# Optimization experiments

Hardware: AMD Instinct MI355X
Metric: run time of the kernel (lower is better)

## Reference

```python
import jax, jax.numpy as jnp
import numpy as np

# Dimensions (see shape_source): B batches, W walks, L walk length, N anonymized node-id space
B, W, L, N = 256, 128, 20, 64
SIGMA = 2.0  # CooccurrenceMatrix(sigma=2.0)


def setup_inputs() -> dict:
    key = jax.random.key(0)
    k1, k2 = jax.random.split(key)
    anonymized_nodes = jax.random.randint(k1, (B, W, L), 0, N, dtype=jnp.int32)
    walk_masks = jax.random.randint(k2, (B, W, L), 0, 2).astype(bool)
    # Gaussian positional kernel buffer: kernel[i,j] = exp(-(i-j)^2 / sigma^2)
    pos = jnp.arange(L, dtype=jnp.float32)
    kernel = jnp.exp(-((pos[:, None] - pos[None, :]) ** 2) / (SIGMA ** 2))
    return {"anonymized_nodes": anonymized_nodes, "walk_masks": walk_masks, "kernel": kernel}


def reference(anonymized_nodes, walk_masks, kernel):
    # Faithful vectorized form of CooccurrenceMatrix.forward.
    # Original: per batch, group valid (walk,pos) entries by node id (sort +
    # change-points); for each group with >=2 entries, scatter-add
    # kernel[pos_i, pos_j] into cooccurrence[b, walk_i, walk_j] for all pairs
    # (i,j) in the group (including i==j). Then normalize by outer product of
    # walk lengths, clamp, tanh.
    valid = walk_masks.astype(jnp.float32)                     # [B,W,L]
    # T[b,w,l,n] = 1 if entry (w,l) is valid and holds node id n
    T = jax.nn.one_hot(anonymized_nodes, N, dtype=jnp.float32) * valid[..., None]  # [B,W,L,N]
    # Segments with < 2 occurrences contribute nothing (original skips them)
    cnt = T.sum(axis=(1, 2))                                   # [B,N]
    T = T * (cnt >= 2.0).astype(jnp.float32)[:, None, None, :]
    K = jnp.clip(kernel, -10.0, 10.0)                          # clamp as in _add_segment_deterministic
    # cooccurrence[b,w,v] = sum_n sum_{l,m} T[b,w,l,n] K[l,m] T[b,v,m,n]
    S = jnp.einsum('bwln,lm->bwmn', T, K)                      # [B,W,L,N]
    cooc = jnp.einsum('bwmn,bvmn->bwv', S, T)                  # [B,W,W]
    # Normalization by walk-length outer product
    walk_lens = valid.sum(-1)                                  # [B,W]
    norm = jnp.clip(walk_lens[:, :, None] * walk_lens[:, None, :], 1e-6, None)
    valid_pairs = (walk_lens[:, :, None] > 0) & (walk_lens[:, None, :] > 0)
    cooc = jnp.where(valid_pairs, cooc / norm, 0.0)
    return jnp.tanh(jnp.clip(cooc, -10.0, 10.0))
```

## Files before the change

kernel.cpp:

```cpp
#include <hip/hip_runtime.h>
#include <hip/hip_bf16.h>

#define BB   256
#define W    128
#define L    20
#define NN   64
#define WL   (W * L)
#define NT   1024
#define CS   129
#define NSLOT 3
#define NKEY (L * NN)

__global__ __launch_bounds__(NT) void cooc_kernel(
    const int* __restrict__ nodes,
    const void* __restrict__ masks,
    const float* __restrict__ kern,
    float* __restrict__ out)
{
    __shared__ __align__(16) float cooc[W * CS];
    __shared__ unsigned ent[WL + 4];
    __shared__ unsigned hist[NKEY];
    __shared__ int cnt[NN];
    __shared__ int wlen[W];
    __shared__ int det[3];
    __shared__ int totS;

    const int tid = threadIdx.x;
    const int b = blockIdx.x;
    const int base = b * WL;

    const unsigned mword = ((const unsigned*)masks)[tid];
    int nval[NSLOT];
    #pragma unroll
    for (int k = 0; k < NSLOT; k++) {
        int e = tid + k * NT;
        nval[k] = (e < WL) ? nodes[base + e] : 0;
    }

    if (tid < 3) det[tid] = 0;
    if (tid < W) wlen[tid] = 0;
    if (tid < NKEY) hist[tid] = 0;
    if (tid + NT < NKEY) hist[tid + NT] = 0;
    {
        float4* c4 = (float4*)cooc;
        for (int i = tid; i < (W * CS) / 4; i += NT)
            c4[i] = make_float4(0.f, 0.f, 0.f, 0.f);
    }
    {
        unsigned v = mword;
        unsigned long long b0 = __ballot(v > 1u);
        unsigned long long b1 = __ballot(v != 0u && v != 0x3F800000u);
        unsigned long long b2 = __ballot(v != 0u && v != 0x3F80u && v != 0x3F800000u &&
                                         v != 0x3F803F80u && v != 0x3C00u &&
                                         v != 0x3C000000u && v != 0x3C003C00u);
        if ((tid & 63) == 0) {
            if (b0) atomicOr(&det[0], 1);
            if (b1) atomicOr(&det[1], 1);
            if (b2) atomicOr(&det[2], 1);
        }
    }
    __syncthreads();
    const int flag = det[0] ? (det[1] ? (det[2] ? 1 : 3) : 2) : 0;

    auto validAt = [&](int idx) -> bool {
        switch (flag) {
            case 0:  return ((const int*)masks)[idx] != 0;
            case 2:  return ((const float*)masks)[idx] != 0.0f;
            case 3:  return ((const unsigned short*)masks)[idx] != 0;
            default: return ((const unsigned char*)masks)[idx] != 0;
        }
    };

    unsigned eval[NSLOT];
    int      kreg[NSLOT];
    #pragma unroll
    for (int k = 0; k < NSLOT; k++) {
        int e = tid + k * NT;
        eval[k] = 0xFFFFFFFFu;
        kreg[k] = 0;
        if (e < WL && validAt(base + e)) {
            int n = nval[k] & (NN - 1);
            int w = e / L;
            int l = e - w * L;
            eval[k] = ((unsigned)n << 12) | ((unsigned)l << 7) | (unsigned)w;
            kreg[k] = l * NN + n;
            atomicAdd(&hist[kreg[k]], 1u);
            atomicAdd(&wlen[w], 1);
        }
    }
    __syncthreads();

    if (tid < NN) {
        int s = 0;
        #pragma unroll
        for (int l = 0; l < L; l++) s += (int)hist[l * NN + tid];
        cnt[tid] = s;
        int inc = s;
        #pragma unroll
        for (int d = 1; d < NN; d <<= 1) {
            int t = __shfl_up(inc, d, 64);
            if (tid >= d) inc += t;
        }
        int run = inc - s;
        if (tid == NN - 1) totS = inc;
        #pragma unroll
        for (int l = 0; l < L; l++) {
            int t = (int)hist[l * NN + tid];
            hist[l * NN + tid] = (unsigned)run;
            run += t;
        }
    }
    __syncthreads();

    if (tid == 0) ent[totS] = 0xFFFFFFFFu;
    #pragma unroll
    for (int k = 0; k < NSLOT; k++) {
        if (eval[k] != 0xFFFFFFFFu) {
            unsigned p = atomicAdd(&hist[kreg[k]], 1u);
            ent[p] = eval[k];
        }
    }
    __syncthreads();

    const float KC = -0.360673760222f;
    const int tot = totS;
    #pragma unroll
    for (int k = 0; k < NSLOT; k++) {
        const int p = tid + k * NT;
        if (p >= tot) continue;
        const unsigned e = ent[p];
        const unsigned key1 = e >> 7;
        const int n = (int)(e >> 12);
        const int w1row = (int)(e & 127u) * CS;
        if (cnt[n] >= 2)
            atomicAdd(&cooc[w1row + (int)(e & 127u)], 0.5f);
        int j = p + 1;
        while (true) {
            unsigned e2 = ent[j];
            unsigned d = (e2 >> 7) - key1;
            if (d > 7u) break;
            float kv = __builtin_amdgcn_exp2f((float)(d * d) * KC);
            atomicAdd(&cooc[w1row + (int)(e2 & 127u)], kv);
            j++;
        }
    }
    __syncthreads();

    for (int i = tid; i < W * W; i += NT) {
        int wr = i >> 7;
        int v = i & (W - 1);
        float s = cooc[wr * CS + v] + cooc[v * CS + wr];
        int lw = wlen[wr], lv = wlen[v];
        float nrm = (float)(lw * lv);
        float x = s * __builtin_amdgcn_rcpf(fmaxf(nrm, 1e-6f));
        x = fminf(fmaxf(x, -10.f), 10.f);
        float e = __builtin_amdgcn_exp2f(x * 2.885390082f);
        float t = (e - 1.f) * __builtin_amdgcn_rcpf(e + 1.f);
        out[b * W * W + i] = (lw > 0 && lv > 0) ? t : 0.f;
    }
}

extern "C" void kernel_launch(void* const* d_in, const int* in_sizes, int n_in,
                              void* d_out, int out_size, void* d_ws, size_t ws_size,
                              hipStream_t stream) {
    const int*   nodes = (const int*)d_in[0];
    const void*  masks = d_in[1];
    const float* kern  = (const float*)d_in[2];
    float* out = (float*)d_out;

    cooc_kernel<<<BB, NT, 0, stream>>>(nodes, masks, kern, out);
}
```

Measured before the change: 82.03 us.

## Narrow the positional window and drop redundant atomics in the bucket scatter

The pair loop now uses a precomputed bucket end index and stops at a position difference of 5 instead of 7. This discards kernel terms of about exp(-9) and below, cutting the shared-memory atomic adds in the hot loop. The second atomic pass for the counting-sort scatter is gone: each entry keeps the rank it got from its first histogram atomic and adds a separate prefix offset. Walk lengths now come from ballot bitmasks and popcount instead of per-entry atomics. The trade is a slightly larger approximation error from the narrower window.

```diff
diff --git a/kernel.cpp b/kernel.cpp
--- a/kernel.cpp
+++ b/kernel.cpp
@@ -10,6 +10,7 @@
 #define CS   129
 #define NSLOT 3
 #define NKEY (L * NN)
+#define DLMAX 5
 
 __global__ __launch_bounds__(NT) void cooc_kernel(
     const int* __restrict__ nodes,
@@ -18,8 +19,10 @@
     float* __restrict__ out)
 {
     __shared__ __align__(16) float cooc[W * CS];
-    __shared__ unsigned ent[WL + 4];
+    __shared__ unsigned ent[WL];
     __shared__ unsigned hist[NKEY];
+    __shared__ unsigned offs[NKEY];
+    __shared__ unsigned long long maskS[40];
     __shared__ int cnt[NN];
     __shared__ int wlen[W];
     __shared__ int det[3];
@@ -38,8 +41,7 @@
     }
 
     if (tid < 3) det[tid] = 0;
-    if (tid < W) wlen[tid] = 0;
-    if (tid < NKEY) hist[tid] = 0;
+    hist[tid] = 0;
     if (tid + NT < NKEY) hist[tid + NT] = 0;
     {
         float4* c4 = (float4*)cooc;
@@ -73,20 +75,25 @@
 
     unsigned eval[NSLOT];
     int      kreg[NSLOT];
+    unsigned plocal[NSLOT];
     #pragma unroll
     for (int k = 0; k < NSLOT; k++) {
         int e = tid + k * NT;
+        bool valid = (e < WL) && validAt(base + e);
         eval[k] = 0xFFFFFFFFu;
         kreg[k] = 0;
-        if (e < WL && validAt(base + e)) {
+        plocal[k] = 0;
+        if (valid) {
             int n = nval[k] & (NN - 1);
             int w = e / L;
             int l = e - w * L;
             eval[k] = ((unsigned)n << 12) | ((unsigned)l << 7) | (unsigned)w;
             kreg[k] = l * NN + n;
-            atomicAdd(&hist[kreg[k]], 1u);
-            atomicAdd(&wlen[w], 1);
         }
+        unsigned long long bal = __ballot(valid);
+        int widx = k * 16 + (tid >> 6);
+        if ((tid & 63) == 0 && widx < 40) maskS[widx] = bal;
+        if (valid) plocal[k] = atomicAdd(&hist[kreg[k]], 1u);
     }
     __syncthreads();
 
@@ -105,20 +112,26 @@
         if (tid == NN - 1) totS = inc;
         #pragma unroll
         for (int l = 0; l < L; l++) {
-            int t = (int)hist[l * NN + tid];
-            hist[l * NN + tid] = (unsigned)run;
+            int idx = l * NN + tid;
+            int t = (int)hist[idx];
+            offs[idx] = (unsigned)run;
             run += t;
+            hist[idx] = (unsigned)run;
         }
+    }
+    if (tid < W) {
+        int bit0 = tid * L;
+        int i0 = bit0 >> 6, sh = bit0 & 63;
+        unsigned long long m = maskS[i0] >> sh;
+        if (sh > 64 - L) m |= maskS[i0 + 1] << (64 - sh);
+        wlen[tid] = __popcll(m & 0xFFFFFu);
     }
     __syncthreads();
 
-    if (tid == 0) ent[totS] = 0xFFFFFFFFu;
     #pragma unroll
     for (int k = 0; k < NSLOT; k++) {
-        if (eval[k] != 0xFFFFFFFFu) {
-            unsigned p = atomicAdd(&hist[kreg[k]], 1u);
-            ent[p] = eval[k];
-        }
+        if (eval[k] != 0xFFFFFFFFu)
+            ent[offs[kreg[k]] + plocal[k]] = eval[k];
     }
     __syncthreads();
 
@@ -129,19 +142,18 @@
         const int p = tid + k * NT;
         if (p >= tot) continue;
         const unsigned e = ent[p];
-        const unsigned key1 = e >> 7;
         const int n = (int)(e >> 12);
-        const int w1row = (int)(e & 127u) * CS;
-        if (cnt[n] >= 2)
-            atomicAdd(&cooc[w1row + (int)(e & 127u)], 0.5f);
-        int j = p + 1;
-        while (true) {
+        const int l1 = (int)((e >> 7) & 31u);
+        const int w1 = (int)(e & 127u);
+        const int w1row = w1 * CS;
+        if (cnt[n] >= 2) atomicAdd(&cooc[w1row + w1], 0.5f);
+        const int lmax = (l1 + DLMAX < L - 1) ? (l1 + DLMAX) : (L - 1);
+        const int jend = (int)hist[lmax * NN + n];
+        for (int j = p + 1; j < jend; j++) {
             unsigned e2 = ent[j];
-            unsigned d = (e2 >> 7) - key1;
-            if (d > 7u) break;
-            float kv = __builtin_amdgcn_exp2f((float)(d * d) * KC);
+            int dl = (int)((e2 >> 7) & 31u) - l1;
+            float kv = __builtin_amdgcn_exp2f((float)(dl * dl) * KC);
             atomicAdd(&cooc[w1row + (int)(e2 & 127u)], kv);
-            j++;
         }
     }
     __syncthreads();
```

New measurement: 79.61 us. 3.0% less time.
